# Kernel optimization log

Measured on AMD Instinct MI355X. Metric: run time of the kernel, lower is better.

Reference implementation:

```python
import jax, jax.numpy as jnp
import numpy as np

B, S, D = 2, 2048, 1024
H = 16
HD = D // H  # 64


def setup_inputs() -> dict:
    key = jax.random.key(0)
    ks = jax.random.split(key, 6)
    std = 1.0 / np.sqrt(D)
    x = jax.random.normal(ks[0], (B, S, D), dtype=jnp.float32)
    Wq = jax.random.uniform(ks[1], (D, D), jnp.float32, -std, std)
    Wk = jax.random.uniform(ks[2], (D, D), jnp.float32, -std, std)
    Wv = jax.random.uniform(ks[3], (D, D), jnp.float32, -std, std)
    Wo = jax.random.uniform(ks[4], (D, D), jnp.float32, -std, std)
    bo = jax.random.uniform(ks[5], (D,), jnp.float32, -std, std)
    return {"x": x, "Wq": Wq, "Wk": Wk, "Wv": Wv, "Wo": Wo, "bo": bo}


def reference(x, Wq, Wk, Wv, Wo, bo):
    b, n, _ = x.shape
    # project and split heads: [b, H, n, HD]
    def split_heads(y):
        return y.reshape(b, n, H, HD).transpose(0, 2, 1, 3)
    q = split_heads(jnp.einsum('bnd,ed->bne', x, Wq))
    k = split_heads(jnp.einsum('bnd,ed->bne', x, Wk))
    v = split_heads(jnp.einsum('bnd,ed->bne', x, Wv))
    scores = jnp.einsum('bhqd,bhkd->bhqk', q, k)
    causal = jnp.triu(jnp.ones((n, n), dtype=bool), k=1)
    # original masks with -inf BEFORE scaling; -inf/scale == -inf so math matches
    scores = jnp.where(causal, -jnp.inf, scores) / jnp.sqrt(jnp.asarray(HD, scores.dtype))
    attn = jax.nn.softmax(scores, axis=-1)
    ctx = jnp.einsum('bhqk,bhkd->bhqd', attn, v)
    ctx = ctx.transpose(0, 2, 1, 3).reshape(b, n, D)
    return jnp.einsum('bnd,ed->bne', ctx, Wo) + bo
```

## Files before the change

kernel.cpp:

```cpp
#include <hip/hip_runtime.h>

#define DEV __device__ __forceinline__

typedef __bf16 bf16x8 __attribute__((ext_vector_type(8)));
typedef float f32x4 __attribute__((ext_vector_type(4)));
typedef float f32x16 __attribute__((ext_vector_type(16)));
typedef unsigned u32x4 __attribute__((ext_vector_type(4)));

constexpr int S_LEN = 2048;
constexpr int DMODEL = 1024;
constexpr int NHEAD = 16;
constexpr int HDIM = 64;
constexpr int BATCH = 2;
constexpr int MROWS = BATCH * S_LEN;
constexpr float QSCALE = 0.125f * 1.44269504088896f;

DEV short f2bf(float x) {
  unsigned u = __builtin_bit_cast(unsigned, x);
  unsigned r = u + 0x7fffu + ((u >> 16) & 1u);
  return (short)(r >> 16);
}

#define MFMA16(a, b, c) __builtin_amdgcn_mfma_f32_16x16x32_bf16((a), (b), (c), 0, 0, 0)
#define MFMA32(a, b, c) __builtin_amdgcn_mfma_f32_32x32x16_bf16((a), (b), (c), 0, 0, 0)
#define GLL16(g, l)                                                                     \
  __builtin_amdgcn_global_load_lds((const __attribute__((address_space(1))) void*)(g),  \
                                   (__attribute__((address_space(3))) void*)(l), 16, 0, 0)

DEV unsigned cvt_pk_bf16(float a, float b) {
  unsigned r;
  asm("v_cvt_pk_bf16_f32 %0, %1, %2" : "=v"(r) : "v"(a), "v"(b));
  return r;
}
DEV void swap32(unsigned& a, unsigned& b) {
  asm("v_permlane32_swap_b32 %0, %1" : "+v"(a), "+v"(b));
}

__global__ void cvt_kernel(const float* __restrict__ in, short* __restrict__ out, int n) {
  int i = (blockIdx.x * blockDim.x + threadIdx.x) * 4;
  const int stride = gridDim.x * blockDim.x * 4;
  for (; i < n; i += stride) {
    float4 v = *(const float4*)&in[i];
    short4 r;
    r.x = f2bf(v.x);
    r.y = f2bf(v.y);
    r.z = f2bf(v.z);
    r.w = f2bf(v.w);
    *(short4*)&out[i] = r;
  }
}

__global__ void cvt_w4(const float* __restrict__ Wq, const float* __restrict__ Wk,
                       const float* __restrict__ Wv, const float* __restrict__ Wo,
                       short* __restrict__ out) {
  const float* src = blockIdx.y == 0 ? Wq : blockIdx.y == 1 ? Wk : blockIdx.y == 2 ? Wv : Wo;
  short* dst = out + (size_t)blockIdx.y * (DMODEL * DMODEL);
  int i = (blockIdx.x * blockDim.x + threadIdx.x) * 4;
  const int stride = gridDim.x * blockDim.x * 4;
  for (; i < DMODEL * DMODEL; i += stride) {
    float4 v = *(const float4*)&src[i];
    short4 r;
    r.x = f2bf(v.x);
    r.y = f2bf(v.y);
    r.z = f2bf(v.z);
    r.w = f2bf(v.w);
    *(short4*)&dst[i] = r;
  }
}

__global__ __launch_bounds__(256) void gemm_bt(const short* __restrict__ A,
                                               const short* __restrict__ Bt,
                                               short* __restrict__ outb) {
  constexpr int K = DMODEL;
  constexpr size_t XN = (size_t)MROWS * DMODEL;
  __shared__ short As[2][128 * 64];
  __shared__ short Bs[2][128 * 64];
  const int tid = threadIdx.x;
  const int w = tid >> 6, l = tid & 63;
  const int lr = l & 15, lh = l >> 4;
  const int wr = w >> 1, wc = w & 1;
  const int tm = blockIdx.x, tn = blockIdx.y;
  const bool vswap = (tn >= 16);

  const int srow = tid >> 3;
  const int ssl = tid & 7;
  const int ssg = ssl ^ (srow & 7);

  f32x4 acc[4][4] = {};

#define GSTAGE(KT, BUF)                                                             \
  {                                                                                 \
    _Pragma("unroll") for (int i = 0; i < 4; ++i) {                                 \
      const int row = i * 32 + srow;                                                \
      GLL16(A + (size_t)(tm * 128 + row) * K + (KT)*64 + ssg * 8,                   \
            &As[BUF][(i * 256 + w * 64) * 8]);                                      \
    }                                                                               \
    _Pragma("unroll") for (int i = 0; i < 4; ++i) {                                 \
      const int row = i * 32 + srow;                                                \
      GLL16(Bt + (size_t)(tn * 128 + row) * K + (KT)*64 + ssg * 8,                  \
            &Bs[BUF][(i * 256 + w * 64) * 8]);                                      \
    }                                                                               \
  }

  GSTAGE(0, 0);
  asm volatile("s_waitcnt vmcnt(0)" ::: "memory");
  __syncthreads();

  for (int kt = 0; kt < K / 64; ++kt) {
    const int buf = kt & 1;
    if (kt < K / 64 - 1) GSTAGE(kt + 1, buf ^ 1);

#pragma unroll
    for (int kh = 0; kh < 2; ++kh) {
      bf16x8 af[4], bfr[4];
#pragma unroll
      for (int mi = 0; mi < 4; ++mi) {
        const int row = wr * 64 + mi * 16 + lr;
        af[mi] = *(const bf16x8*)&As[buf][row * 64 + 8 * ((kh * 4 + lh) ^ (row & 7))];
      }
#pragma unroll
      for (int ni = 0; ni < 4; ++ni) {
        const int row = wc * 64 + ni * 16 + lr;
        bfr[ni] = *(const bf16x8*)&Bs[buf][row * 64 + 8 * ((kh * 4 + lh) ^ (row & 7))];
      }
      if (vswap) {
#pragma unroll
        for (int mi = 0; mi < 4; ++mi)
#pragma unroll
          for (int ni = 0; ni < 4; ++ni)
            acc[mi][ni] = MFMA16(bfr[ni], af[mi], acc[mi][ni]);
      } else {
#pragma unroll
        for (int mi = 0; mi < 4; ++mi)
#pragma unroll
          for (int ni = 0; ni < 4; ++ni)
            acc[mi][ni] = MFMA16(af[mi], bfr[ni], acc[mi][ni]);
      }
    }

    asm volatile("s_waitcnt vmcnt(0)" ::: "memory");
    __syncthreads();
  }
#undef GSTAGE

  const int m0 = tm * 128 + wr * 64;
  const int n0 = tn * 128 + wc * 64;
  if (vswap) {
#pragma unroll
    for (int mi = 0; mi < 4; ++mi)
#pragma unroll
      for (int ni = 0; ni < 4; ++ni)
#pragma unroll
        for (int i = 0; i < 4; ++i) {
          const int e = n0 + ni * 16 + lh * 4 + i;
          const int m = m0 + mi * 16 + lr;
          const int ecol = e & (DMODEL - 1);
          const int b = m >> 11, n = m & (S_LEN - 1);
          const int h = ecol >> 6, d = ecol & (HDIM - 1);
          (outb + 2 * XN)[((size_t)((b * NHEAD + h) * HDIM + d)) * S_LEN + n] =
              f2bf(acc[mi][ni][i]);
        }
  } else {
    const int sel = tn >> 3;
#pragma unroll
    for (int mi = 0; mi < 4; ++mi)
#pragma unroll
      for (int ni = 0; ni < 4; ++ni)
#pragma unroll
        for (int i = 0; i < 4; ++i) {
          const int m = m0 + mi * 16 + lh * 4 + i;
          const int e = n0 + ni * 16 + lr;
          const int ecol = e & (DMODEL - 1);
          const int b = m >> 11, n = m & (S_LEN - 1);
          const int h = ecol >> 6, d = ecol & (HDIM - 1);
          if (sel == 0)
            outb[((size_t)((b * NHEAD + h) * S_LEN + n)) * HDIM + d] =
                f2bf(acc[mi][ni][i] * QSCALE);
          else
            (outb + XN)[((size_t)((b * NHEAD + h) * S_LEN + n)) * HDIM + d] =
                f2bf(acc[mi][ni][i]);
        }
  }
}

__global__ __launch_bounds__(256) void gemm_out(const short* __restrict__ A,
                                                const short* __restrict__ Bt,
                                                float* __restrict__ outf,
                                                const float* __restrict__ bias) {
  constexpr int K = DMODEL;
  constexpr int N = DMODEL;
  __shared__ short As[2][64 * 64];
  __shared__ short Bs[2][128 * 64];
  const int tid = threadIdx.x;
  const int w = tid >> 6, l = tid & 63;
  const int lr = l & 15, lh = l >> 4;
  const int wc = w;
  const int tm = blockIdx.x, tn = blockIdx.y;

  const int srow = tid >> 3;
  const int ssl = tid & 7;
  const int ssg = ssl ^ (srow & 7);

  f32x4 acc[4][2] = {};

#define OSTAGE(KT, BUF)                                                             \
  {                                                                                 \
    _Pragma("unroll") for (int i = 0; i < 2; ++i) {                                 \
      const int row = i * 32 + srow;                                                \
      GLL16(A + (size_t)(tm * 64 + row) * K + (KT)*64 + ssg * 8,                    \
            &As[BUF][(i * 256 + w * 64) * 8]);                                      \
    }                                                                               \
    _Pragma("unroll") for (int i = 0; i < 4; ++i) {                                 \
      const int row = i * 32 + srow;                                                \
      GLL16(Bt + (size_t)(tn * 128 + row) * K + (KT)*64 + ssg * 8,                  \
            &Bs[BUF][(i * 256 + w * 64) * 8]);                                      \
    }                                                                               \
  }

  OSTAGE(0, 0);
  asm volatile("s_waitcnt vmcnt(0)" ::: "memory");
  __syncthreads();

  for (int kt = 0; kt < K / 64; ++kt) {
    const int buf = kt & 1;
    if (kt < K / 64 - 1) OSTAGE(kt + 1, buf ^ 1);

#pragma unroll
    for (int kh = 0; kh < 2; ++kh) {
      bf16x8 af[4], bfr[2];
#pragma unroll
      for (int mi = 0; mi < 4; ++mi) {
        const int row = mi * 16 + lr;
        af[mi] = *(const bf16x8*)&As[buf][row * 64 + 8 * ((kh * 4 + lh) ^ (row & 7))];
      }
#pragma unroll
      for (int ni = 0; ni < 2; ++ni) {
        const int row = wc * 32 + ni * 16 + lr;
        bfr[ni] = *(const bf16x8*)&Bs[buf][row * 64 + 8 * ((kh * 4 + lh) ^ (row & 7))];
      }
#pragma unroll
      for (int mi = 0; mi < 4; ++mi)
#pragma unroll
        for (int ni = 0; ni < 2; ++ni)
          acc[mi][ni] = MFMA16(af[mi], bfr[ni], acc[mi][ni]);
    }

    asm volatile("s_waitcnt vmcnt(0)" ::: "memory");
    __syncthreads();
  }
#undef OSTAGE

#pragma unroll
  for (int mi = 0; mi < 4; ++mi)
#pragma unroll
    for (int ni = 0; ni < 2; ++ni)
#pragma unroll
      for (int i = 0; i < 4; ++i) {
        const int m = tm * 64 + mi * 16 + lh * 4 + i;
        const int e = tn * 128 + wc * 32 + ni * 16 + lr;
        outf[(size_t)m * N + e] = acc[mi][ni][i] + bias[e];
      }
}

__global__ __launch_bounds__(256) void attn_kernel(const short* __restrict__ Qg,
                                                   const short* __restrict__ Kg,
                                                   const short* __restrict__ Vg,
                                                   short* __restrict__ ctx) {
  __shared__ alignas(16) short KV[4][8192];
  __shared__ float mls[4][32];
  const int tidx = threadIdx.x;
  const int s = tidx >> 6;
  const int l = tidx & 63;
  const int lq = l & 31;
  const int h5 = l >> 5;
  const int bid = blockIdx.x;
  const int xcd = bid & 7;
  const int j = bid >> 3;
  const int bh = xcd * 4 + (j >> 6);
  const int qi = 63 - (j & 63);
  const int qbase = qi * 32;
  const short* Qh = Qg + (size_t)bh * (S_LEN * HDIM);
  const short* Kh = Kg + (size_t)bh * (S_LEN * HDIM);
  const short* Vh = Vg + (size_t)bh * (HDIM * S_LEN);

  short* Kbase = &KV[s][0];
  short* Vbase = &KV[s][4096];
  const int r8 = l >> 3;
  const int sc = l & 7;

  bf16x8 qf[4];
#pragma unroll
  for (int cc = 0; cc < 4; ++cc)
    qf[cc] = *(const bf16x8*)&Qh[(size_t)(qbase + lq) * HDIM + cc * 16 + h5 * 8];

  f32x16 o0 = {}, o1 = {};
  float ll = 0.f;

  const int ntot = qi + 1;
  const int ts = (ntot * s) >> 2;
  const int te = (ntot * (s + 1)) >> 2;

#define STAGE(T, BUF)                                                              \
  {                                                                                \
    _Pragma("unroll") for (int i = 0; i < 4; ++i) {                                \
      const int R = i * 8 + r8;                                                    \
      const int sg = sc ^ (R & 7);                                                 \
      GLL16(Kh + (size_t)((T)*32 + R) * HDIM + sg * 8,                             \
            &Kbase[(BUF)*2048 + i * 512]);                                         \
      GLL16(Vh + (size_t)(2 * R + (sg >> 2)) * S_LEN + (T)*32 + (sg & 3) * 8,      \
            &Vbase[(BUF)*2048 + i * 512]);                                         \
    }                                                                              \
  }

  if (ts < te) STAGE(ts, 0);

  for (int t = ts; t < te; ++t) {
    const int buf = (t - ts) & 1;
    if (t + 1 < te) {
      STAGE(t + 1, buf ^ 1);
      asm volatile("s_waitcnt vmcnt(8)" ::: "memory");
    } else {
      asm volatile("s_waitcnt vmcnt(0)" ::: "memory");
    }
    const short* Ksb = &Kbase[buf * 2048];
    const short* Vsb = &Vbase[buf * 2048];

    bf16x8 kf[4];
#pragma unroll
    for (int cc = 0; cc < 4; ++cc)
      kf[cc] = *(const bf16x8*)&Ksb[lq * 64 + 8 * ((cc * 2 + h5) ^ (lq & 7))];
    f32x16 st = {};
    __builtin_amdgcn_s_setprio(1);
#pragma unroll
    for (int cc = 0; cc < 4; ++cc) st = MFMA32(kf[cc], qf[cc], st);
    __builtin_amdgcn_s_setprio(0);

    if (t == qi) {
#pragma unroll
      for (int rr = 0; rr < 16; ++rr) {
        const int crow = (rr & 3) + 8 * (rr >> 2) + 4 * h5;
        if (crow > lq) st[rr] = -__builtin_inff();
      }
    }

#pragma unroll
    for (int rr = 0; rr < 16; ++rr) {
      st[rr] = __builtin_amdgcn_exp2f(st[rr]);
      ll += st[rr];
    }

    unsigned a0 = cvt_pk_bf16(st[0], st[1]), b0 = cvt_pk_bf16(st[4], st[5]);
    unsigned a1 = cvt_pk_bf16(st[2], st[3]), b1 = cvt_pk_bf16(st[6], st[7]);
    unsigned a2 = cvt_pk_bf16(st[8], st[9]), b2 = cvt_pk_bf16(st[12], st[13]);
    unsigned a3 = cvt_pk_bf16(st[10], st[11]), b3 = cvt_pk_bf16(st[14], st[15]);
    swap32(a0, b0);
    swap32(a1, b1);
    swap32(a2, b2);
    swap32(a3, b3);
    const u32x4 pw0 = {a0, a1, b0, b1};
    const u32x4 pw1 = {a2, a3, b2, b3};
    const bf16x8 pa0 = __builtin_bit_cast(bf16x8, pw0);
    const bf16x8 pa1 = __builtin_bit_cast(bf16x8, pw1);

    const int R0 = lq >> 1, p0 = (lq & 1) * 4 + h5;
    const int R1 = 16 + (lq >> 1);
    const bf16x8 v00 = *(const bf16x8*)&Vsb[R0 * 64 + 8 * ((p0 + 0) ^ (R0 & 7))];
    const bf16x8 v01 = *(const bf16x8*)&Vsb[R0 * 64 + 8 * ((p0 + 2) ^ (R0 & 7))];
    const bf16x8 v10 = *(const bf16x8*)&Vsb[R1 * 64 + 8 * ((p0 + 0) ^ (R1 & 7))];
    const bf16x8 v11 = *(const bf16x8*)&Vsb[R1 * 64 + 8 * ((p0 + 2) ^ (R1 & 7))];
    __builtin_amdgcn_s_setprio(1);
    o0 = MFMA32(pa0, v00, o0);
    o1 = MFMA32(pa0, v10, o1);
    o0 = MFMA32(pa1, v01, o0);
    o1 = MFMA32(pa1, v11, o1);
    __builtin_amdgcn_s_setprio(0);
  }
#undef STAGE

  float* me = (float*)&KV[s][0];
#pragma unroll
  for (int rr = 0; rr < 16; ++rr) {
    const int crow = (rr & 3) + 8 * (rr >> 2) + 4 * h5;
    me[crow * 64 + lq] = o0[rr];
    me[crow * 64 + 32 + lq] = o1[rr];
  }
  ll += __shfl_xor(ll, 32);
  if (h5 == 0) mls[s][lq] = ll;
  __syncthreads();

  const float* om0 = (const float*)&KV[0][0];
  const float* om1 = (const float*)&KV[1][0];
  const float* om2 = (const float*)&KV[2][0];
  const float* om3 = (const float*)&KV[3][0];
  const int b = bh >> 4, h = bh & (NHEAD - 1);
  const int r2 = tidx >> 3;
  const int d0 = (tidx & 7) * 8;
  const float inv =
      __builtin_amdgcn_rcpf(mls[0][r2] + mls[1][r2] + mls[2][r2] + mls[3][r2]);
  const size_t base = (size_t)(b * S_LEN + qbase + r2) * DMODEL + h * HDIM + d0;
#pragma unroll
  for (int i = 0; i < 8; ++i) {
    const int o = r2 * 64 + d0 + i;
    const float v = (om0[o] + om1[o] + om2[o] + om3[o]) * inv;
    ctx[base + i] = f2bf(v);
  }
}

extern "C" void kernel_launch(void* const* d_in, const int* in_sizes, int n_in,
                              void* d_out, int out_size, void* d_ws, size_t ws_size,
                              hipStream_t stream) {
  const float* x = (const float*)d_in[0];
  const float* Wq = (const float*)d_in[1];
  const float* Wk = (const float*)d_in[2];
  const float* Wv = (const float*)d_in[3];
  const float* Wo = (const float*)d_in[4];
  const float* bo = (const float*)d_in[5];

  const size_t XN = (size_t)MROWS * DMODEL;
  const size_t WN = (size_t)DMODEL * DMODEL;

  short* ws = (short*)d_ws;
  short* xb = ws;
  short* Wqb = xb + XN;
  short* Wob = Wqb + 3 * WN;
  short* Qb = Wob + WN;
  short* Kb = Qb + XN;
  short* Vb = Kb + XN;
  short* ctxb = Vb + XN;
  if (ws_size < (5 * XN + 4 * WN) * sizeof(short)) return;

  cvt_kernel<<<2048, 256, 0, stream>>>(x, xb, (int)XN);
  cvt_w4<<<dim3(256, 4), 256, 0, stream>>>(Wq, Wk, Wv, Wo, Wqb);

  gemm_bt<<<dim3(MROWS / 128, 3 * DMODEL / 128), 256, 0, stream>>>(xb, Wqb, Qb);

  attn_kernel<<<2048, 256, 0, stream>>>(Qb, Kb, Vb, ctxb);

  gemm_out<<<dim3(MROWS / 64, DMODEL / 128), 256, 0, stream>>>(ctxb, Wob, (float*)d_out,
                                                               bo);
}
```

Baseline: 118.5 us.

## Load V tiles directly into registers and halve attention LDS footprint

```diff
diff --git a/kernel.cpp b/kernel.cpp
--- a/kernel.cpp
+++ b/kernel.cpp
@@ -266,7 +266,7 @@
                                                    const short* __restrict__ Kg,
                                                    const short* __restrict__ Vg,
                                                    short* __restrict__ ctx) {
-  __shared__ alignas(16) short KV[4][8192];
+  __shared__ alignas(16) short KV[4][4096];
   __shared__ float mls[4][32];
   const int tidx = threadIdx.x;
   const int s = tidx >> 6;
@@ -284,7 +284,6 @@
   const short* Vh = Vg + (size_t)bh * (HDIM * S_LEN);
 
   short* Kbase = &KV[s][0];
-  short* Vbase = &KV[s][4096];
   const int r8 = l >> 3;
   const int sc = l & 7;
 
@@ -300,82 +299,93 @@
   const int ts = (ntot * s) >> 2;
   const int te = (ntot * (s + 1)) >> 2;
 
-#define STAGE(T, BUF)                                                              \
+#define KSTAGE(T, BUF)                                                             \
   {                                                                                \
     _Pragma("unroll") for (int i = 0; i < 4; ++i) {                                \
       const int R = i * 8 + r8;                                                    \
       const int sg = sc ^ (R & 7);                                                 \
       GLL16(Kh + (size_t)((T)*32 + R) * HDIM + sg * 8,                             \
             &Kbase[(BUF)*2048 + i * 512]);                                         \
-      GLL16(Vh + (size_t)(2 * R + (sg >> 2)) * S_LEN + (T)*32 + (sg & 3) * 8,      \
-            &Vbase[(BUF)*2048 + i * 512]);                                         \
     }                                                                              \
   }
 
-  if (ts < te) STAGE(ts, 0);
-
-  for (int t = ts; t < te; ++t) {
-    const int buf = (t - ts) & 1;
+#define VLOAD(T, V0, V1, V2, V3)                                \
+  {                                                             \
+    const short* Vt = Vh + (size_t)lq * S_LEN + (T)*32;         \
+    V0 = *(const bf16x8*)&Vt[h5 * 8];                           \
+    V1 = *(const bf16x8*)&Vt[(h5 + 2) * 8];                     \
+    V2 = *(const bf16x8*)&Vt[32 * S_LEN + h5 * 8];              \
+    V3 = *(const bf16x8*)&Vt[32 * S_LEN + (h5 + 2) * 8];        \
+  }
+
+#define COMPUTE(T, KSB, V0, V1, V2, V3)                                              \
+  do {                                                                               \
+    const short* Ksb = (KSB);                                                        \
+    bf16x8 kf[4];                                                                    \
+    _Pragma("unroll") for (int cc = 0; cc < 4; ++cc)                                 \
+        kf[cc] = *(const bf16x8*)&Ksb[lq * 64 + 8 * ((cc * 2 + h5) ^ (lq & 7))];     \
+    f32x16 st = {};                                                                  \
+    __builtin_amdgcn_s_setprio(1);                                                   \
+    _Pragma("unroll") for (int cc = 0; cc < 4; ++cc) st = MFMA32(kf[cc], qf[cc], st);\
+    __builtin_amdgcn_s_setprio(0);                                                   \
+    if ((T) == qi) {                                                                 \
+      _Pragma("unroll") for (int rr = 0; rr < 16; ++rr) {                            \
+        const int crow = (rr & 3) + 8 * (rr >> 2) + 4 * h5;                          \
+        if (crow > lq) st[rr] = -__builtin_inff();                                   \
+      }                                                                              \
+    }                                                                                \
+    _Pragma("unroll") for (int rr = 0; rr < 16; ++rr) {                              \
+      st[rr] = __builtin_amdgcn_exp2f(st[rr]);                                       \
+      ll += st[rr];                                                                  \
+    }                                                                                \
+    unsigned a0 = cvt_pk_bf16(st[0], st[1]), b0 = cvt_pk_bf16(st[4], st[5]);         \
+    unsigned a1 = cvt_pk_bf16(st[2], st[3]), b1 = cvt_pk_bf16(st[6], st[7]);         \
+    unsigned a2 = cvt_pk_bf16(st[8], st[9]), b2 = cvt_pk_bf16(st[12], st[13]);       \
+    unsigned a3 = cvt_pk_bf16(st[10], st[11]), b3 = cvt_pk_bf16(st[14], st[15]);     \
+    swap32(a0, b0);                                                                  \
+    swap32(a1, b1);                                                                  \
+    swap32(a2, b2);                                                                  \
+    swap32(a3, b3);                                                                  \
+    const u32x4 pw0 = {a0, a1, b0, b1};                                              \
+    const u32x4 pw1 = {a2, a3, b2, b3};                                              \
+    const bf16x8 pa0 = __builtin_bit_cast(bf16x8, pw0);                              \
+    const bf16x8 pa1 = __builtin_bit_cast(bf16x8, pw1);                              \
+    __builtin_amdgcn_s_setprio(1);                                                   \
+    o0 = MFMA32(pa0, V0, o0);                                                        \
+    o1 = MFMA32(pa0, V2, o1);                                                        \
+    o0 = MFMA32(pa1, V1, o0);                                                        \
+    o1 = MFMA32(pa1, V3, o1);                                                        \
+    __builtin_amdgcn_s_setprio(0);                                                   \
+  } while (0)
+
+  bf16x8 vA0, vA1, vA2, vA3, vB0, vB1, vB2, vB3;
+  if (ts < te) {
+    KSTAGE(ts, 0);
+    VLOAD(ts, vA0, vA1, vA2, vA3);
+  }
+  for (int t = ts; t < te; t += 2) {
     if (t + 1 < te) {
-      STAGE(t + 1, buf ^ 1);
+      KSTAGE(t + 1, 1);
+      VLOAD(t + 1, vB0, vB1, vB2, vB3);
       asm volatile("s_waitcnt vmcnt(8)" ::: "memory");
     } else {
       asm volatile("s_waitcnt vmcnt(0)" ::: "memory");
     }
-    const short* Ksb = &Kbase[buf * 2048];
-    const short* Vsb = &Vbase[buf * 2048];
-
-    bf16x8 kf[4];
-#pragma unroll
-    for (int cc = 0; cc < 4; ++cc)
-      kf[cc] = *(const bf16x8*)&Ksb[lq * 64 + 8 * ((cc * 2 + h5) ^ (lq & 7))];
-    f32x16 st = {};
-    __builtin_amdgcn_s_setprio(1);
-#pragma unroll
-    for (int cc = 0; cc < 4; ++cc) st = MFMA32(kf[cc], qf[cc], st);
-    __builtin_amdgcn_s_setprio(0);
-
-    if (t == qi) {
-#pragma unroll
-      for (int rr = 0; rr < 16; ++rr) {
-        const int crow = (rr & 3) + 8 * (rr >> 2) + 4 * h5;
-        if (crow > lq) st[rr] = -__builtin_inff();
-      }
+    COMPUTE(t, &Kbase[0], vA0, vA1, vA2, vA3);
+    if (t + 1 < te) {
+      if (t + 2 < te) {
+        KSTAGE(t + 2, 0);
+        VLOAD(t + 2, vA0, vA1, vA2, vA3);
+        asm volatile("s_waitcnt vmcnt(8)" ::: "memory");
+      } else {
+        asm volatile("s_waitcnt vmcnt(0)" ::: "memory");
+      }
+      COMPUTE(t + 1, &Kbase[2048], vB0, vB1, vB2, vB3);
     }
-
-#pragma unroll
-    for (int rr = 0; rr < 16; ++rr) {
-      st[rr] = __builtin_amdgcn_exp2f(st[rr]);
-      ll += st[rr];
-    }
-
-    unsigned a0 = cvt_pk_bf16(st[0], st[1]), b0 = cvt_pk_bf16(st[4], st[5]);
-    unsigned a1 = cvt_pk_bf16(st[2], st[3]), b1 = cvt_pk_bf16(st[6], st[7]);
-    unsigned a2 = cvt_pk_bf16(st[8], st[9]), b2 = cvt_pk_bf16(st[12], st[13]);
-    unsigned a3 = cvt_pk_bf16(st[10], st[11]), b3 = cvt_pk_bf16(st[14], st[15]);
-    swap32(a0, b0);
-    swap32(a1, b1);
-    swap32(a2, b2);
-    swap32(a3, b3);
-    const u32x4 pw0 = {a0, a1, b0, b1};
-    const u32x4 pw1 = {a2, a3, b2, b3};
-    const bf16x8 pa0 = __builtin_bit_cast(bf16x8, pw0);
-    const bf16x8 pa1 = __builtin_bit_cast(bf16x8, pw1);
-
-    const int R0 = lq >> 1, p0 = (lq & 1) * 4 + h5;
-    const int R1 = 16 + (lq >> 1);
-    const bf16x8 v00 = *(const bf16x8*)&Vsb[R0 * 64 + 8 * ((p0 + 0) ^ (R0 & 7))];
-    const bf16x8 v01 = *(const bf16x8*)&Vsb[R0 * 64 + 8 * ((p0 + 2) ^ (R0 & 7))];
-    const bf16x8 v10 = *(const bf16x8*)&Vsb[R1 * 64 + 8 * ((p0 + 0) ^ (R1 & 7))];
-    const bf16x8 v11 = *(const bf16x8*)&Vsb[R1 * 64 + 8 * ((p0 + 2) ^ (R1 & 7))];
-    __builtin_amdgcn_s_setprio(1);
-    o0 = MFMA32(pa0, v00, o0);
-    o1 = MFMA32(pa0, v10, o1);
-    o0 = MFMA32(pa1, v01, o0);
-    o1 = MFMA32(pa1, v11, o1);
-    __builtin_amdgcn_s_setprio(0);
-  }
-#undef STAGE
+  }
+#undef KSTAGE
+#undef VLOAD
+#undef COMPUTE
 
   float* me = (float*)&KV[s][0];
 #pragma unroll
```

Result: slower. 122.3 us (+3.1%).
